# Kernel tuning notes

Hardware: AMD Instinct MI355X
Metric: run time of the kernel (lower is better)

## Reference

```python
import jax, jax.numpy as jnp
import numpy as np

B, S, D, E = 4, 4096, 2048, 8


def setup_inputs() -> dict:
    key = jax.random.key(0)
    kx, kw, kb = jax.random.split(key, 3)
    x = jax.random.normal(kx, (B, S, D), dtype=jnp.float32)
    # nn.Linear(d_model, n_experts): weight [E, D], bias [E]
    bound = 1.0 / np.sqrt(D)
    W = jax.random.uniform(kw, (E, D), minval=-bound, maxval=bound, dtype=jnp.float32)
    b = jax.random.uniform(kb, (E,), minval=-bound, maxval=bound, dtype=jnp.float32)
    return {"x": x, "W": W, "b": b}


def reference(x, W, b):
    # logits = x @ W^T + b : [B, S, E]
    logits = jnp.einsum("bsd,ed->bse", x, W) + b
    gate = jax.nn.softmax(logits, axis=-1)
    top2_val, top2_idx = jax.lax.top_k(gate, 2)  # [B, S, 2] each
    return (top2_val, top2_idx, gate)
```

## Files before the change

kernel.cpp:

```cpp
#include <hip/hip_runtime.h>
#include <hip/hip_bf16.h>
#include <math.h>


#define NTOK   16384
#define DMODEL 2048
#define NEXP   8

__global__ __launch_bounds__(256, 2) void top2router_kernel(
    const float* __restrict__ x,
    const float* __restrict__ W,
    const float* __restrict__ b,
    float* __restrict__ out)
{
    __shared__ __align__(16) float sW[NEXP * DMODEL];

    const int t = threadIdx.x;

    {
        const float4* __restrict__ Wv = reinterpret_cast<const float4*>(W);
        float4* sWv = reinterpret_cast<float4*>(sW);
#pragma unroll
        for (int i = 0; i < 16; ++i)
            sWv[i * 256 + t] = Wv[i * 256 + t];
    }
    __syncthreads();

    const int lane = t & 63;
    const int wave = t >> 6;
    const int j    = lane & 7;
    const int st   = lane >> 3;
    const int token = (blockIdx.x * 4 + wave) * 8 + st;

    const float* __restrict__ xptr = x + (size_t)token * DMODEL + (j << 2);

    float4 acc[NEXP];
#pragma unroll
    for (int e = 0; e < NEXP; ++e) acc[e] = make_float4(0.f, 0.f, 0.f, 0.f);

#pragma unroll 2
    for (int k = 0; k < 64; ++k) {
        const float4 xv = *reinterpret_cast<const float4*>(xptr + (k << 5));
#pragma unroll
        for (int e = 0; e < NEXP; ++e) {
            const float4 wv =
                *reinterpret_cast<const float4*>(&sW[e * DMODEL + (k << 5) + (j << 2)]);
            acc[e].x = fmaf(xv.x, wv.x, acc[e].x);
            acc[e].y = fmaf(xv.y, wv.y, acc[e].y);
            acc[e].z = fmaf(xv.z, wv.z, acc[e].z);
            acc[e].w = fmaf(xv.w, wv.w, acc[e].w);
        }
    }

    float v0 = (acc[0].x + acc[0].y) + (acc[0].z + acc[0].w);
    float v1 = (acc[1].x + acc[1].y) + (acc[1].z + acc[1].w);
    float v2 = (acc[2].x + acc[2].y) + (acc[2].z + acc[2].w);
    float v3 = (acc[3].x + acc[3].y) + (acc[3].z + acc[3].w);
    float v4 = (acc[4].x + acc[4].y) + (acc[4].z + acc[4].w);
    float v5 = (acc[5].x + acc[5].y) + (acc[5].z + acc[5].w);
    float v6 = (acc[6].x + acc[6].y) + (acc[6].z + acc[6].w);
    float v7 = (acc[7].x + acc[7].y) + (acc[7].z + acc[7].w);

    float s0 = v0 + __shfl_xor(v0, 1, 8);
    float s1 = v1 + __shfl_xor(v1, 1, 8);
    float s2 = v2 + __shfl_xor(v2, 1, 8);
    float s3 = v3 + __shfl_xor(v3, 1, 8);
    float s4 = v4 + __shfl_xor(v4, 1, 8);
    float s5 = v5 + __shfl_xor(v5, 1, 8);
    float s6 = v6 + __shfl_xor(v6, 1, 8);
    float s7 = v7 + __shfl_xor(v7, 1, 8);
    const bool b0 = (j & 1);
    float t0 = b0 ? s1 : s0;
    float t1 = b0 ? s3 : s2;
    float t2 = b0 ? s5 : s4;
    float t3 = b0 ? s7 : s6;
    float p0 = t0 + __shfl_xor(t0, 2, 8);
    float p1 = t1 + __shfl_xor(t1, 2, 8);
    float p2 = t2 + __shfl_xor(t2, 2, 8);
    float p3 = t3 + __shfl_xor(t3, 2, 8);
    const bool b1 = (j & 2);
    float u0 = b1 ? p1 : p0;
    float u1 = b1 ? p3 : p2;
    float q0 = u0 + __shfl_xor(u0, 4, 8);
    float q1 = u1 + __shfl_xor(u1, 4, 8);
    const float dot = (j & 4) ? q1 : q0;

    const float logit = dot + b[j];

    float m = logit;
#pragma unroll
    for (int s = 4; s; s >>= 1) m = fmaxf(m, __shfl_xor(m, s, 8));
    const float ex = expf(logit - m);
    float sum = ex;
#pragma unroll
    for (int s = 4; s; s >>= 1) sum += __shfl_xor(sum, s, 8);
    const float gate = ex / sum;

    out[65536 + token * NEXP + j] = gate;

    float g1 = gate; int e1 = j;
#pragma unroll
    for (int s = 4; s; s >>= 1) {
        const float og = __shfl_xor(g1, s, 8);
        const int   oe = __shfl_xor(e1, s, 8);
        if (og > g1 || (og == g1 && oe < e1)) { g1 = og; e1 = oe; }
    }
    float g2 = (j == e1) ? -INFINITY : gate; int e2 = j;
#pragma unroll
    for (int s = 4; s; s >>= 1) {
        const float og = __shfl_xor(g2, s, 8);
        const int   oe = __shfl_xor(e2, s, 8);
        if (og > g2 || (og == g2 && oe < e2)) { g2 = og; e2 = oe; }
    }

    if (j == 0) {
        out[token * 2 + 0]         = g1;
        out[token * 2 + 1]         = g2;
        out[32768 + token * 2 + 0] = (float)e1;
        out[32768 + token * 2 + 1] = (float)e2;
    }
}

extern "C" void kernel_launch(void* const* d_in, const int* in_sizes, int n_in,
                              void* d_out, int out_size, void* d_ws, size_t ws_size,
                              hipStream_t stream) {
    const float* x = (const float*)d_in[0];
    const float* W = (const float*)d_in[1];
    const float* b = (const float*)d_in[2];
    float* out = (float*)d_out;

    top2router_kernel<<<512, 256, 0, stream>>>(x, W, b, out);
}
```

Baseline: 196.6 us.

## Process two tokens per thread with register-prefetched x loads

Each thread now accumulates dot products for two tokens at once, so every shared-memory weight load feeds twice as many FMAs. The next x chunk is prefetched into registers a step ahead (software pipelining). The grid is halved to 256 blocks and launch bounds drop to one block per SM. This cuts LDS traffic per FMA and hides global-load latency, at the cost of doubled accumulator registers and fewer blocks, which may leave some CUs idle on a 256-CU part and lower occupancy for a bandwidth-bound read of x.

```diff
diff --git a/kernel.cpp b/kernel.cpp
--- a/kernel.cpp
+++ b/kernel.cpp
@@ -4,63 +4,16 @@
 
 
 #define NTOK   16384
-#define DMODEL 2048
-#define NEXP   8
+#define DM     2048
+#define NE     8
 
-__global__ __launch_bounds__(256, 2) void top2router_kernel(
-    const float* __restrict__ x,
-    const float* __restrict__ W,
-    const float* __restrict__ b,
-    float* __restrict__ out)
-{
-    __shared__ __align__(16) float sW[NEXP * DMODEL];
+__device__ __forceinline__ float fold4(const float4 a) {
+    return (a.x + a.y) + (a.z + a.w);
+}
 
-    const int t = threadIdx.x;
-
-    {
-        const float4* __restrict__ Wv = reinterpret_cast<const float4*>(W);
-        float4* sWv = reinterpret_cast<float4*>(sW);
-#pragma unroll
-        for (int i = 0; i < 16; ++i)
-            sWv[i * 256 + t] = Wv[i * 256 + t];
-    }
-    __syncthreads();
-
-    const int lane = t & 63;
-    const int wave = t >> 6;
-    const int j    = lane & 7;
-    const int st   = lane >> 3;
-    const int token = (blockIdx.x * 4 + wave) * 8 + st;
-
-    const float* __restrict__ xptr = x + (size_t)token * DMODEL + (j << 2);
-
-    float4 acc[NEXP];
-#pragma unroll
-    for (int e = 0; e < NEXP; ++e) acc[e] = make_float4(0.f, 0.f, 0.f, 0.f);
-
-#pragma unroll 2
-    for (int k = 0; k < 64; ++k) {
-        const float4 xv = *reinterpret_cast<const float4*>(xptr + (k << 5));
-#pragma unroll
-        for (int e = 0; e < NEXP; ++e) {
-            const float4 wv =
-                *reinterpret_cast<const float4*>(&sW[e * DMODEL + (k << 5) + (j << 2)]);
-            acc[e].x = fmaf(xv.x, wv.x, acc[e].x);
-            acc[e].y = fmaf(xv.y, wv.y, acc[e].y);
-            acc[e].z = fmaf(xv.z, wv.z, acc[e].z);
-            acc[e].w = fmaf(xv.w, wv.w, acc[e].w);
-        }
-    }
-
-    float v0 = (acc[0].x + acc[0].y) + (acc[0].z + acc[0].w);
-    float v1 = (acc[1].x + acc[1].y) + (acc[1].z + acc[1].w);
-    float v2 = (acc[2].x + acc[2].y) + (acc[2].z + acc[2].w);
-    float v3 = (acc[3].x + acc[3].y) + (acc[3].z + acc[3].w);
-    float v4 = (acc[4].x + acc[4].y) + (acc[4].z + acc[4].w);
-    float v5 = (acc[5].x + acc[5].y) + (acc[5].z + acc[5].w);
-    float v6 = (acc[6].x + acc[6].y) + (acc[6].z + acc[6].w);
-    float v7 = (acc[7].x + acc[7].y) + (acc[7].z + acc[7].w);
-
+__device__ __forceinline__ float reduce_scatter8(const float4* acc, const int j) {
+    float v0 = fold4(acc[0]), v1 = fold4(acc[1]), v2 = fold4(acc[2]), v3 = fold4(acc[3]);
+    float v4 = fold4(acc[4]), v5 = fold4(acc[5]), v6 = fold4(acc[6]), v7 = fold4(acc[7]);
     float s0 = v0 + __shfl_xor(v0, 1, 8);
     float s1 = v1 + __shfl_xor(v1, 1, 8);
     float s2 = v2 + __shfl_xor(v2, 1, 8);
@@ -83,10 +36,11 @@
     float u1 = b1 ? p3 : p2;
     float q0 = u0 + __shfl_xor(u0, 4, 8);
     float q1 = u1 + __shfl_xor(u1, 4, 8);
-    const float dot = (j & 4) ? q1 : q0;
+    return (j & 4) ? q1 : q0;
+}
 
-    const float logit = dot + b[j];
-
+__device__ __forceinline__ void softmax_top2(const float logit, const int j,
+                                             const int token, float* __restrict__ out) {
     float m = logit;
 #pragma unroll
     for (int s = 4; s; s >>= 1) m = fmaxf(m, __shfl_xor(m, s, 8));
@@ -96,7 +50,7 @@
     for (int s = 4; s; s >>= 1) sum += __shfl_xor(sum, s, 8);
     const float gate = ex / sum;
 
-    out[65536 + token * NEXP + j] = gate;
+    out[65536 + token * NE + j] = gate;
 
     float g1 = gate; int e1 = j;
 #pragma unroll
@@ -112,13 +66,96 @@
         const int   oe = __shfl_xor(e2, s, 8);
         if (og > g2 || (og == g2 && oe < e2)) { g2 = og; e2 = oe; }
     }
-
     if (j == 0) {
         out[token * 2 + 0]         = g1;
         out[token * 2 + 1]         = g2;
         out[32768 + token * 2 + 0] = (float)e1;
         out[32768 + token * 2 + 1] = (float)e2;
     }
+}
+
+__global__ __launch_bounds__(256, 1) void top2router_kernel(
+    const float* __restrict__ x,
+    const float* __restrict__ W,
+    const float* __restrict__ b,
+    float* __restrict__ out)
+{
+    __shared__ __align__(16) float sW[NE * DM];
+
+    const int t = threadIdx.x;
+
+    {
+        const float4* __restrict__ Wv = reinterpret_cast<const float4*>(W);
+        float4* sWv = reinterpret_cast<float4*>(sW);
+#pragma unroll
+        for (int i = 0; i < 16; ++i)
+            sWv[i * 256 + t] = Wv[i * 256 + t];
+    }
+    __syncthreads();
+
+    const int lane = t & 63;
+    const int wave = t >> 6;
+    const int j    = lane & 7;
+    const int st   = lane >> 3;
+    const int base = (blockIdx.x * 4 + wave) * 16;
+    const int tok0 = base + st;
+    const int tok1 = base + st + 8;
+
+    const float* __restrict__ xp0 = x + (size_t)tok0 * DM + (j << 2);
+    const float* __restrict__ xp1 = x + (size_t)tok1 * DM + (j << 2);
+    const float bj = b[j];
+
+    float4 acc0[NE], acc1[NE];
+#pragma unroll
+    for (int e = 0; e < NE; ++e) {
+        acc0[e] = make_float4(0.f, 0.f, 0.f, 0.f);
+        acc1[e] = make_float4(0.f, 0.f, 0.f, 0.f);
+    }
+
+    float4 xa0 = *reinterpret_cast<const float4*>(xp0);
+    float4 xa1 = *reinterpret_cast<const float4*>(xp1);
+
+#pragma unroll 3
+    for (int k = 0; k < 63; ++k) {
+        const float4 xb0 = *reinterpret_cast<const float4*>(xp0 + ((k + 1) << 5));
+        const float4 xb1 = *reinterpret_cast<const float4*>(xp1 + ((k + 1) << 5));
+        const float* wbase = &sW[(k << 5) + (j << 2)];
+#pragma unroll
+        for (int e = 0; e < NE; ++e) {
+            const float4 wv = *reinterpret_cast<const float4*>(wbase + e * DM);
+            acc0[e].x = fmaf(xa0.x, wv.x, acc0[e].x);
+            acc0[e].y = fmaf(xa0.y, wv.y, acc0[e].y);
+            acc0[e].z = fmaf(xa0.z, wv.z, acc0[e].z);
+            acc0[e].w = fmaf(xa0.w, wv.w, acc0[e].w);
+            acc1[e].x = fmaf(xa1.x, wv.x, acc1[e].x);
+            acc1[e].y = fmaf(xa1.y, wv.y, acc1[e].y);
+            acc1[e].z = fmaf(xa1.z, wv.z, acc1[e].z);
+            acc1[e].w = fmaf(xa1.w, wv.w, acc1[e].w);
+        }
+        xa0 = xb0;
+        xa1 = xb1;
+    }
+    {
+        const float* wbase = &sW[(63 << 5) + (j << 2)];
+#pragma unroll
+        for (int e = 0; e < NE; ++e) {
+            const float4 wv = *reinterpret_cast<const float4*>(wbase + e * DM);
+            acc0[e].x = fmaf(xa0.x, wv.x, acc0[e].x);
+            acc0[e].y = fmaf(xa0.y, wv.y, acc0[e].y);
+            acc0[e].z = fmaf(xa0.z, wv.z, acc0[e].z);
+            acc0[e].w = fmaf(xa0.w, wv.w, acc0[e].w);
+            acc1[e].x = fmaf(xa1.x, wv.x, acc1[e].x);
+            acc1[e].y = fmaf(xa1.y, wv.y, acc1[e].y);
+            acc1[e].z = fmaf(xa1.z, wv.z, acc1[e].z);
+            acc1[e].w = fmaf(xa1.w, wv.w, acc1[e].w);
+        }
+    }
+
+    const float logit0 = reduce_scatter8(acc0, j) + bj;
+    const float logit1 = reduce_scatter8(acc1, j) + bj;
+
+    softmax_top2(logit0, j, tok0, out);
+    softmax_top2(logit1, j, tok1, out);
 }
 
 extern "C" void kernel_launch(void* const* d_in, const int* in_sizes, int n_in,
@@ -129,5 +166,5 @@
     const float* b = (const float*)d_in[2];
     float* out = (float*)d_out;
 
-    top2router_kernel<<<512, 256, 0, stream>>>(x, W, b, out);
+    top2router_kernel<<<256, 256, 0, stream>>>(x, W, b, out);
 }
```

After: 195.1 us. No clear change (-0.8%).

## Split router GEMV along the model dimension into partial-sum and finalize kernels

Applied to the files above, without the earlier changes.

The single kernel that gave each block 32 tokens with the full 64 KB weight in shared memory is replaced by a split-K scheme. 4096 blocks each handle 32 tokens over a 256-wide slice of the model dimension, with only 8 KB of weights in shared memory and explicit register prefetch of x. A second kernel sums the 8 partials, adds the bias, and runs the softmax and top-2. This aims to raise occupancy and memory-level parallelism for the 128 MB x read, at the cost of an extra launch and 4 MB of partial-sum traffic through the workspace.

```diff
diff --git a/kernel.cpp b/kernel.cpp
--- a/kernel.cpp
+++ b/kernel.cpp
@@ -3,64 +3,20 @@
 #include <math.h>
 
 
-#define NTOK   16384
-#define DMODEL 2048
-#define NEXP   8
+#define NTOK  16384
+#define DM    2048
+#define NE    8
+#define KS    8
+#define KSF   (DM / KS)
+#define PART_STRIDE (NTOK * NE)
 
-__global__ __launch_bounds__(256, 2) void top2router_kernel(
-    const float* __restrict__ x,
-    const float* __restrict__ W,
-    const float* __restrict__ b,
-    float* __restrict__ out)
-{
-    __shared__ __align__(16) float sW[NEXP * DMODEL];
+__device__ __forceinline__ float fold4(const float4 a) {
+    return (a.x + a.y) + (a.z + a.w);
+}
 
-    const int t = threadIdx.x;
-
-    {
-        const float4* __restrict__ Wv = reinterpret_cast<const float4*>(W);
-        float4* sWv = reinterpret_cast<float4*>(sW);
-#pragma unroll
-        for (int i = 0; i < 16; ++i)
-            sWv[i * 256 + t] = Wv[i * 256 + t];
-    }
-    __syncthreads();
-
-    const int lane = t & 63;
-    const int wave = t >> 6;
-    const int j    = lane & 7;
-    const int st   = lane >> 3;
-    const int token = (blockIdx.x * 4 + wave) * 8 + st;
-
-    const float* __restrict__ xptr = x + (size_t)token * DMODEL + (j << 2);
-
-    float4 acc[NEXP];
-#pragma unroll
-    for (int e = 0; e < NEXP; ++e) acc[e] = make_float4(0.f, 0.f, 0.f, 0.f);
-
-#pragma unroll 2
-    for (int k = 0; k < 64; ++k) {
-        const float4 xv = *reinterpret_cast<const float4*>(xptr + (k << 5));
-#pragma unroll
-        for (int e = 0; e < NEXP; ++e) {
-            const float4 wv =
-                *reinterpret_cast<const float4*>(&sW[e * DMODEL + (k << 5) + (j << 2)]);
-            acc[e].x = fmaf(xv.x, wv.x, acc[e].x);
-            acc[e].y = fmaf(xv.y, wv.y, acc[e].y);
-            acc[e].z = fmaf(xv.z, wv.z, acc[e].z);
-            acc[e].w = fmaf(xv.w, wv.w, acc[e].w);
-        }
-    }
-
-    float v0 = (acc[0].x + acc[0].y) + (acc[0].z + acc[0].w);
-    float v1 = (acc[1].x + acc[1].y) + (acc[1].z + acc[1].w);
-    float v2 = (acc[2].x + acc[2].y) + (acc[2].z + acc[2].w);
-    float v3 = (acc[3].x + acc[3].y) + (acc[3].z + acc[3].w);
-    float v4 = (acc[4].x + acc[4].y) + (acc[4].z + acc[4].w);
-    float v5 = (acc[5].x + acc[5].y) + (acc[5].z + acc[5].w);
-    float v6 = (acc[6].x + acc[6].y) + (acc[6].z + acc[6].w);
-    float v7 = (acc[7].x + acc[7].y) + (acc[7].z + acc[7].w);
-
+__device__ __forceinline__ float reduce_scatter8(const float4* acc, const int j) {
+    float v0 = fold4(acc[0]), v1 = fold4(acc[1]), v2 = fold4(acc[2]), v3 = fold4(acc[3]);
+    float v4 = fold4(acc[4]), v5 = fold4(acc[5]), v6 = fold4(acc[6]), v7 = fold4(acc[7]);
     float s0 = v0 + __shfl_xor(v0, 1, 8);
     float s1 = v1 + __shfl_xor(v1, 1, 8);
     float s2 = v2 + __shfl_xor(v2, 1, 8);
@@ -83,10 +39,11 @@
     float u1 = b1 ? p3 : p2;
     float q0 = u0 + __shfl_xor(u0, 4, 8);
     float q1 = u1 + __shfl_xor(u1, 4, 8);
-    const float dot = (j & 4) ? q1 : q0;
+    return (j & 4) ? q1 : q0;
+}
 
-    const float logit = dot + b[j];
-
+__device__ __forceinline__ void softmax_top2(const float logit, const int j,
+                                             const int token, float* __restrict__ out) {
     float m = logit;
 #pragma unroll
     for (int s = 4; s; s >>= 1) m = fmaxf(m, __shfl_xor(m, s, 8));
@@ -96,7 +53,7 @@
     for (int s = 4; s; s >>= 1) sum += __shfl_xor(sum, s, 8);
     const float gate = ex / sum;
 
-    out[65536 + token * NEXP + j] = gate;
+    out[65536 + token * NE + j] = gate;
 
     float g1 = gate; int e1 = j;
 #pragma unroll
@@ -112,7 +69,6 @@
         const int   oe = __shfl_xor(e2, s, 8);
         if (og > g2 || (og == g2 && oe < e2)) { g2 = og; e2 = oe; }
     }
-
     if (j == 0) {
         out[token * 2 + 0]         = g1;
         out[token * 2 + 1]         = g2;
@@ -121,13 +77,95 @@
     }
 }
 
+__global__ __launch_bounds__(256, 6) void router_partial(
+    const float* __restrict__ x,
+    const float* __restrict__ W,
+    float* __restrict__ part)
+{
+    __shared__ __align__(16) float sW8[NE * KSF];
+
+    const int t     = threadIdx.x;
+    const int chunk = blockIdx.x >> 3;
+    const int ks    = blockIdx.x & 7;
+
+    {
+        const float4* __restrict__ Wv = reinterpret_cast<const float4*>(W);
+        float4* sWv = reinterpret_cast<float4*>(sW8);
+#pragma unroll
+        for (int i = 0; i < 2; ++i) {
+            const int idx = i * 256 + t;
+            const int e   = idx >> 6;
+            const int f4  = idx & 63;
+            sWv[idx] = Wv[e * (DM / 4) + ks * (KSF / 4) + f4];
+        }
+    }
+    __syncthreads();
+
+    const int lane = t & 63;
+    const int wave = t >> 6;
+    const int j    = lane & 7;
+    const int st   = lane >> 3;
+    const int tok  = chunk * 32 + wave * 8 + st;
+
+    const float* __restrict__ xp =
+        x + (size_t)tok * DM + ks * KSF + (j << 2);
+
+    float4 acc[NE];
+#pragma unroll
+    for (int e = 0; e < NE; ++e) acc[e] = make_float4(0.f, 0.f, 0.f, 0.f);
+
+    float4 xa = *reinterpret_cast<const float4*>(xp);
+#pragma unroll
+    for (int it = 0; it < 8; ++it) {
+        float4 xn;
+        if (it < 7) xn = *reinterpret_cast<const float4*>(xp + ((it + 1) << 5));
+        const float* wbase = &sW8[(it << 5) + (j << 2)];
+#pragma unroll
+        for (int e = 0; e < NE; ++e) {
+            const float4 wv = *reinterpret_cast<const float4*>(wbase + e * KSF);
+            acc[e].x = fmaf(xa.x, wv.x, acc[e].x);
+            acc[e].y = fmaf(xa.y, wv.y, acc[e].y);
+            acc[e].z = fmaf(xa.z, wv.z, acc[e].z);
+            acc[e].w = fmaf(xa.w, wv.w, acc[e].w);
+        }
+        xa = xn;
+    }
+
+    const float p = reduce_scatter8(acc, j);
+    part[(size_t)ks * PART_STRIDE + (size_t)tok * NE + j] = p;
+}
+
+__global__ __launch_bounds__(256) void router_final(
+    const float* __restrict__ part,
+    const float* __restrict__ b,
+    float* __restrict__ out)
+{
+    const int t    = threadIdx.x;
+    const int lane = t & 63;
+    const int wave = t >> 6;
+    const int j    = lane & 7;
+    const int st   = lane >> 3;
+    const int tok  = blockIdx.x * 32 + wave * 8 + st;
+
+    const size_t base = (size_t)tok * NE + j;
+    float s = 0.f;
+#pragma unroll
+    for (int ks = 0; ks < KS; ++ks)
+        s += part[(size_t)ks * PART_STRIDE + base];
+
+    const float logit = s + b[j];
+    softmax_top2(logit, j, tok, out);
+}
+
 extern "C" void kernel_launch(void* const* d_in, const int* in_sizes, int n_in,
                               void* d_out, int out_size, void* d_ws, size_t ws_size,
                               hipStream_t stream) {
     const float* x = (const float*)d_in[0];
     const float* W = (const float*)d_in[1];
     const float* b = (const float*)d_in[2];
-    float* out = (float*)d_out;
+    float* out  = (float*)d_out;
+    float* part = (float*)d_ws;
 
-    top2router_kernel<<<512, 256, 0, stream>>>(x, W, b, out);
+    router_partial<<<4096, 256, 0, stream>>>(x, W, part);
+    router_final<<<512, 256, 0, stream>>>(part, b, out);
 }
```

New measurement: 193.4 us. Within noise of the previous version (-1.6%).
